# Performance work log

Measured on AMD Instinct MI355X. Metric: run time of the kernel, lower is better.

The kernel has to match this reference:

```python
import jax, jax.numpy as jnp
import numpy as np

BS, CHAN, H, W = 2, 128, 1, 900

def setup_inputs() -> dict:
    key = jax.random.key(0)
    k1, k2 = jax.random.split(key)
    encoded_l = jax.random.normal(k1, (BS, CHAN, H, W), dtype=jnp.float32)
    encoded_r = jax.random.normal(k2, (BS, CHAN, H, W), dtype=jnp.float32)
    return {"encoded_l": encoded_l, "encoded_r": encoded_r}

def reference(encoded_l, encoded_r):
    # Original torch code (h must be 1 for shapes to align):
    #   tiled_l[b,c,i,j] = l[b,c,0,j]  (rows are copies of l)
    #   tiled_r[b,c,i,j] = r[b,c,0,i]  (cols are copies of r)
    #   diff = |tiled_l - tiled_r|  -> (bs, chan, w, w)
    bs, chan, h, w = encoded_l.shape
    l = encoded_l.reshape(bs, chan, h * w)  # (bs, chan, w)
    r = encoded_r.reshape(bs, chan, h * w)
    # broadcasted all-pairs abs difference (cost volume), no explicit tiling
    diff = jnp.abs(l[:, :, None, :] - r[:, :, :, None])  # (bs, chan, w, w)
    return diff
```

## Files before the change

### kernel.cpp

```cpp
#include <hip/hip_runtime.h>


#define BS    2
#define CHAN  128
#define W     900
#define W4    225
#define TILE4 (W * W4)
#define SPLIT 4
#define PART  (TILE4 / SPLIT)

typedef float v4f __attribute__((ext_vector_type(4)));

__global__ __launch_bounds__(256, 4)
void deltaLayer_57294863728910_kernel(const float* __restrict__ l,
                                      const float* __restrict__ r,
                                      float* __restrict__ out) {
    __shared__ float sl[W];
    __shared__ float sr[W];

    const int bc   = blockIdx.x >> 2;
    const int part = blockIdx.x & (SPLIT - 1);

    const float* lrow = l + bc * W;
    const float* rrow = r + bc * W;
    for (int t = threadIdx.x; t < W; t += 256) {
        sl[t] = lrow[t];
        sr[t] = rrow[t];
    }
    __syncthreads();

    v4f* out4 = (v4f*)out + (size_t)bc * TILE4;

    const int kbeg = part * PART + threadIdx.x;
    const int kend = (part + 1) * PART;
    for (int k = kbeg; k < kend; k += 256) {
        int i  = k / W4;
        int j4 = k - i * W4;
        float rv = sr[i];
        v4f   lv = *(const v4f*)&sl[j4 * 4];
        v4f   o;
        o.x = fabsf(lv.x - rv);
        o.y = fabsf(lv.y - rv);
        o.z = fabsf(lv.z - rv);
        o.w = fabsf(lv.w - rv);
        __builtin_nontemporal_store(o, &out4[k]);
    }
}

extern "C" void kernel_launch(void* const* d_in, const int* in_sizes, int n_in,
                              void* d_out, int out_size, void* d_ws, size_t ws_size,
                              hipStream_t stream) {
    const float* l = (const float*)d_in[0];
    const float* r = (const float*)d_in[1];
    float* out = (float*)d_out;

    dim3 grid(BS * CHAN * SPLIT);
    dim3 block(256);
    deltaLayer_57294863728910_kernel<<<grid, block, 0, stream>>>(l, r, out);
}
```

Measured before the change: 871.7 us.

## Assign each thread a column quad across row chunks, dropping LDS and division

Each block now covers 50 rows of one batch-channel slice; each thread holds its four l values in registers and loops over rows, reading r directly from global memory. This removes the shared-memory staging, barrier, and per-element integer divide/modulo. Stores change from nontemporal to regular, and the launch bound is raised to allow more resident blocks. About 31 of 256 threads per block sit idle.

```diff
diff --git a/kernel.cpp b/kernel.cpp
--- a/kernel.cpp
+++ b/kernel.cpp
@@ -6,44 +6,34 @@
 #define W     900
 #define W4    225
 #define TILE4 (W * W4)
-#define SPLIT 4
-#define PART  (TILE4 / SPLIT)
+#define SPLIT 18
+#define ROWS  50
 
 typedef float v4f __attribute__((ext_vector_type(4)));
 
-__global__ __launch_bounds__(256, 4)
+__global__ __launch_bounds__(256, 8)
 void deltaLayer_57294863728910_kernel(const float* __restrict__ l,
                                       const float* __restrict__ r,
                                       float* __restrict__ out) {
-    __shared__ float sl[W];
-    __shared__ float sr[W];
+    const int bc = blockIdx.y;
+    const int i0 = blockIdx.x * ROWS;
+    const int t  = threadIdx.x;
+    if (t >= W4) return;
 
-    const int bc   = blockIdx.x >> 2;
-    const int part = blockIdx.x & (SPLIT - 1);
+    const v4f lv = ((const v4f*)(l + bc * W))[t];
+    const float* rp = r + bc * W + i0;
 
-    const float* lrow = l + bc * W;
-    const float* rrow = r + bc * W;
-    for (int t = threadIdx.x; t < W; t += 256) {
-        sl[t] = lrow[t];
-        sr[t] = rrow[t];
-    }
-    __syncthreads();
+    v4f* ob = (v4f*)out + (size_t)bc * TILE4 + (size_t)i0 * W4 + t;
 
-    v4f* out4 = (v4f*)out + (size_t)bc * TILE4;
-
-    const int kbeg = part * PART + threadIdx.x;
-    const int kend = (part + 1) * PART;
-    for (int k = kbeg; k < kend; k += 256) {
-        int i  = k / W4;
-        int j4 = k - i * W4;
-        float rv = sr[i];
-        v4f   lv = *(const v4f*)&sl[j4 * 4];
-        v4f   o;
+    #pragma unroll 5
+    for (int i = 0; i < ROWS; ++i) {
+        float rv = rp[i];
+        v4f o;
         o.x = fabsf(lv.x - rv);
         o.y = fabsf(lv.y - rv);
         o.z = fabsf(lv.z - rv);
         o.w = fabsf(lv.w - rv);
-        __builtin_nontemporal_store(o, &out4[k]);
+        ob[(size_t)i * W4] = o;
     }
 }
 
@@ -54,7 +44,7 @@
     const float* r = (const float*)d_in[1];
     float* out = (float*)d_out;
 
-    dim3 grid(BS * CHAN * SPLIT);
+    dim3 grid(SPLIT, BS * CHAN);
     dim3 block(256);
     deltaLayer_57294863728910_kernel<<<grid, block, 0, stream>>>(l, r, out);
 }
```

Measured after the change: 828.2 us. -5.0%, faster.
